# Kernel optimization log

Hardware: AMD Instinct MI355X
Metric: run time of the kernel (lower is better)

Reference implementation:

```python
import jax, jax.numpy as jnp
import numpy as np

D = 256; H = 8; DK = D // H
NA = 100000; NP_ = 100000; E = 400000
EPS = 1e-5


def _seg_softmax(s, seg, n):
    # destination-grouped (dst-normalized) edge softmax, per head
    m = jax.ops.segment_max(s, seg, num_segments=n)
    ex = jnp.exp(s - m[seg])
    den = jax.ops.segment_sum(ex, seg, num_segments=n)
    return ex / den[seg]


def setup_inputs() -> dict:
    key = jax.random.key(0)
    ks = jax.random.split(key, 16)
    sc = 1.0 / np.sqrt(D)
    sck = 1.0 / np.sqrt(DK)
    return {
        "h_author": jax.random.normal(ks[0], (NA, D), jnp.float32),
        "h_paper": jax.random.normal(ks[1], (NP_, D), jnp.float32),
        "writes_src": jax.random.randint(ks[2], (E,), 0, NA),
        "writes_dst": jax.random.randint(ks[3], (E,), 0, NP_),
        "wb_src": jax.random.randint(ks[4], (E,), 0, NP_),
        "wb_dst": jax.random.randint(ks[5], (E,), 0, NA),
        "cites_src": jax.random.randint(ks[6], (E,), 0, NP_),
        "cites_dst": jax.random.randint(ks[7], (E,), 0, NP_),
        # per-node-type linear layers, stacked on leading axis [num_node_types=2, ...]
        "Wk": jax.random.normal(ks[8], (2, D, D), jnp.float32) * sc,
        "bk": jnp.zeros((2, D), jnp.float32),
        "Wq": jax.random.normal(ks[9], (2, D, D), jnp.float32) * sc,
        "bq": jnp.zeros((2, D), jnp.float32),
        "Wv": jax.random.normal(ks[10], (2, D, D), jnp.float32) * sc,
        "bv": jnp.zeros((2, D), jnp.float32),
        "Wfc": jax.random.normal(ks[11], (2, D, D), jnp.float32) * sc,
        "bfc": jnp.zeros((2, D), jnp.float32),
        "ln_g": jnp.ones((2, D), jnp.float32),
        "ln_b": jnp.zeros((2, D), jnp.float32),
        # per-edge-type tensors [num_edge_types=3, ...]
        "att_w": jax.random.normal(ks[12], (3, H, DK, DK), jnp.float32) * sck,
        "val_w": jax.random.normal(ks[13], (3, H, DK, DK), jnp.float32) * sck,
        "canon_w": jnp.ones((3, H), jnp.float32),
        "res": jnp.ones((2,), jnp.float32),
    }


def reference(h_author, h_paper, writes_src, writes_dst, wb_src, wb_dst,
              cites_src, cites_dst, Wk, bk, Wq, bq, Wv, bv, Wfc, bfc,
              ln_g, ln_b, att_w, val_w, canon_w, res):
    sqrt_dk = np.float32(np.sqrt(DK))

    def proj(h, W, b):
        return (h @ W + b).reshape(-1, H, DK)  # [N, H, d_k]

    # node type 0 = author, 1 = paper
    k_a, v_a, q_a = proj(h_author, Wk[0], bk[0]), proj(h_author, Wv[0], bv[0]), proj(h_author, Wq[0], bq[0])
    k_p, v_p, q_p = proj(h_paper, Wk[1], bk[1]), proj(h_paper, Wv[1], bv[1]), proj(h_paper, Wq[1], bq[1])

    def etype_agg(q_d, k_s, v_s, src, dst, e, n_dst):
        ke = jnp.einsum('nhd,hde->nhe', k_s, att_w[e])
        ve = jnp.einsum('nhd,hde->nhe', v_s, val_w[e])
        score = jnp.einsum('ehd,ehd->eh', q_d[dst], ke[src]) * canon_w[e] / sqrt_dk  # [E, H]
        a = _seg_softmax(score, dst, n_dst)
        return jax.ops.segment_sum(ve[src] * a[:, :, None], dst, num_segments=n_dst)  # [N_d, H, d_k]

    agg_writes = etype_agg(q_p, k_a, v_a, writes_src, writes_dst, 0, NP_)
    agg_wb = etype_agg(q_a, k_p, v_p, wb_src, wb_dst, 1, NA)
    agg_cites = etype_agg(q_p, k_p, v_p, cites_src, cites_dst, 2, NP_)

    t_author = agg_wb                          # single incoming etype -> mean is identity
    t_paper = 0.5 * (agg_writes + agg_cites)   # cross_reducer='mean' over 2 etypes

    def node_out(t, h, nid):
        alpha = jax.nn.sigmoid(res[nid])
        hp = (t.reshape(-1, D) @ Wfc[nid] + bfc[nid]) * alpha + h * (1.0 - alpha)
        mu = hp.mean(-1, keepdims=True)
        var = ((hp - mu) ** 2).mean(-1, keepdims=True)
        return (hp - mu) / jnp.sqrt(var + EPS) * ln_g[nid] + ln_b[nid]

    return node_out(t_author, h_author, 0), node_out(t_paper, h_paper, 1)
```

## Files before the change

### kernel.cpp

```cpp
#include <hip/hip_runtime.h>
#include <hip/hip_bf16.h>
#include <math.h>

using short8  = __attribute__((ext_vector_type(8))) short;
using ushort8v = __attribute__((ext_vector_type(8))) unsigned short;
using f32x4   = __attribute__((ext_vector_type(4))) float;

__device__ __forceinline__ float bf2f(unsigned short u) {
    return __uint_as_float(((unsigned int)u) << 16);
}
__device__ __forceinline__ unsigned short f2bf(float f) {
    unsigned int x = __float_as_uint(f);
    return (unsigned short)((x + 0x7fffu + ((x >> 16) & 1u)) >> 16);
}
__device__ __forceinline__ void gll16(const void* g, void* l) {
    __builtin_amdgcn_global_load_lds(
        (const __attribute__((address_space(1))) unsigned int*)g,
        (__attribute__((address_space(3))) unsigned int*)l, 16, 0, 0);
}

__global__ __launch_bounds__(256) void build_eff_t(
    const float* __restrict__ Wk, const float* __restrict__ Wv,
    const float* __restrict__ att_w, const float* __restrict__ val_w,
    unsigned short* __restrict__ wt)
{
    int gid = blockIdx.x;
    int mat = gid >> 8, c = gid & 255;
    int e = mat >> 1, which = mat & 1;
    int ts = (e == 0) ? 0 : 1;
    int h = c >> 5, j = c & 31;
    int k = threadIdx.x;
    const float* Wsrc = (which == 0 ? Wk : Wv) + ((size_t)ts * 256 + k) * 256 + h * 32;
    const float* aw = (which == 0 ? att_w : val_w) + (size_t)((e * 8 + h) * 32) * 32 + j;
    float s = 0.f;
    #pragma unroll
    for (int d = 0; d < 32; ++d) s += Wsrc[d] * aw[d * 32];
    int slot = mat < 2 ? mat + 1 : mat + 2;
    wt[((size_t)slot * 256 + c) * 256 + k] = f2bf(s);
}

__global__ void build_eff_bias(
    const float* __restrict__ bk, const float* __restrict__ bv,
    const float* __restrict__ att_w, const float* __restrict__ val_w,
    float* __restrict__ effb)
{
    int mat = blockIdx.x;
    int c = threadIdx.x;
    int e = mat >> 1, which = mat & 1;
    int ts = (e == 0) ? 0 : 1;
    int h = c >> 5, j = c & 31;
    const float* bsrc = (which == 0 ? bk : bv) + ts * 256 + h * 32;
    const float* aw = (which == 0 ? att_w : val_w) + (size_t)((e * 8 + h) * 32) * 32 + j;
    float s = 0.f;
    #pragma unroll
    for (int d = 0; d < 32; ++d) s += bsrc[d] * aw[d * 32];
    effb[mat * 256 + c] = s;
}

__global__ void build_bias_cat(const float* __restrict__ bq,
                               const float* __restrict__ effb,
                               float* __restrict__ bc)
{
    int i = blockIdx.x * 256 + threadIdx.x;
    int seg = i >> 8, o = i & 255;
    float v;
    switch (seg) {
        case 0: v = bq[o]; break;
        case 1: v = effb[o]; break;
        case 2: v = effb[256 + o]; break;
        case 3: v = bq[256 + o]; break;
        case 4: v = effb[512 + o]; break;
        case 5: v = effb[768 + o]; break;
        case 6: v = effb[1024 + o]; break;
        default: v = effb[1280 + o]; break;
    }
    bc[i] = v;
}

__global__ __launch_bounds__(256) void transpose_cast4(
    const float* __restrict__ Wq, const float* __restrict__ Wfc,
    unsigned short* __restrict__ wt)
{
    __shared__ float tile[32][33];
    int mi = blockIdx.x >> 6;
    int bid = blockIdx.x & 63;
    const float* src; int slot;
    switch (mi) {
        case 0: src = Wq;           slot = 0; break;
        case 1: src = Wq + 65536;   slot = 3; break;
        case 2: src = Wfc;          slot = 8; break;
        default: src = Wfc + 65536; slot = 9; break;
    }
    unsigned short* dst = wt + (size_t)slot * 65536;
    int bx = bid & 7, by = bid >> 3;
    int tx = threadIdx.x & 31, ty = threadIdx.x >> 5;
    #pragma unroll
    for (int i = 0; i < 4; ++i)
        tile[ty + i * 8][tx] = src[(size_t)(by * 32 + ty + i * 8) * 256 + bx * 32 + tx];
    __syncthreads();
    #pragma unroll
    for (int i = 0; i < 4; ++i)
        dst[(size_t)(bx * 32 + ty + i * 8) * 256 + by * 32 + tx] = f2bf(tile[tx][ty + i * 8]);
}

__global__ void cast_bf16(const float* __restrict__ in, unsigned short* __restrict__ out, int n4) {
    int i = blockIdx.x * 256 + threadIdx.x;
    if (i < n4) {
        float4 v = ((const float4*)in)[i];
        ushort4 o; o.x = f2bf(v.x); o.y = f2bf(v.y); o.z = f2bf(v.z); o.w = f2bf(v.w);
        ((ushort4*)out)[i] = o;
    }
}

__global__ __launch_bounds__(256, 4) void gemm_cat(
    const unsigned short* __restrict__ A, const unsigned short* __restrict__ Wt,
    const float* __restrict__ bias, unsigned short* __restrict__ C,
    int M, int Ncat)
{
    __shared__ unsigned short As[2][128 * 32];
    __shared__ unsigned short Bs[2][128 * 32];
    int t = threadIdx.x, w = t >> 6, l = t & 63;
    int lr = l & 15, lg = l >> 4;
    int wr = w >> 1, wc = w & 1;
    int m0 = blockIdx.x * 128, n0 = blockIdx.y * 128;

    int lrow = l >> 2, lq = l & 3;
    int qsw = lq ^ ((lrow >> 1) & 3);
    int ar0 = m0 + w * 16 + lrow;        if (ar0 >= M) ar0 = M - 1;
    int ar1 = m0 + (w + 4) * 16 + lrow;  if (ar1 >= M) ar1 = M - 1;
    const unsigned short* Ap0 = A + (size_t)ar0 * 256 + qsw * 8;
    const unsigned short* Ap1 = A + (size_t)ar1 * 256 + qsw * 8;
    const unsigned short* Bp0 = Wt + (size_t)(n0 + w * 16 + lrow) * 256 + qsw * 8;
    const unsigned short* Bp1 = Wt + (size_t)(n0 + (w + 4) * 16 + lrow) * 256 + qsw * 8;

    int aswz = (lg ^ ((lr >> 1) & 3)) * 8;

    f32x4 acc[4][4] = {};

    gll16(Ap0, &As[0][(w * 16) * 32]);
    gll16(Ap1, &As[0][((w + 4) * 16) * 32]);
    gll16(Bp0, &Bs[0][(w * 16) * 32]);
    gll16(Bp1, &Bs[0][((w + 4) * 16) * 32]);
    __syncthreads();

    int cur = 0;
    for (int step = 0; step < 8; ++step) {
        if (step < 7) {
            int k0 = (step + 1) * 32;
            gll16(Ap0 + k0, &As[cur ^ 1][(w * 16) * 32]);
            gll16(Ap1 + k0, &As[cur ^ 1][((w + 4) * 16) * 32]);
            gll16(Bp0 + k0, &Bs[cur ^ 1][(w * 16) * 32]);
            gll16(Bp1 + k0, &Bs[cur ^ 1][((w + 4) * 16) * 32]);
        }
        short8 fa[4], fb[4];
        #pragma unroll
        for (int f = 0; f < 4; ++f) {
            fa[f] = *(const short8*)&As[cur][(wr * 64 + f * 16 + lr) * 32 + aswz];
            fb[f] = *(const short8*)&Bs[cur][(wc * 64 + f * 16 + lr) * 32 + aswz];
        }
        #pragma unroll
        for (int fr = 0; fr < 4; ++fr)
            #pragma unroll
            for (int fc = 0; fc < 4; ++fc)
                acc[fr][fc] = __builtin_amdgcn_mfma_f32_16x16x32_bf16(fa[fr], fb[fc], acc[fr][fc], 0, 0, 0);
        __syncthreads();
        cur ^= 1;
    }

    #pragma unroll
    for (int fr = 0; fr < 4; ++fr) {
        int row = m0 + wr * 64 + fr * 16 + lg * 4;
        #pragma unroll
        for (int fc = 0; fc < 4; ++fc) {
            int col = n0 + wc * 64 + fc * 16 + lr;
            float bv = bias[col];
            #pragma unroll
            for (int ri = 0; ri < 4; ++ri) {
                if (row + ri < M)
                    C[(size_t)(row + ri) * Ncat + col] = f2bf(acc[fr][fc][ri] + bv);
            }
        }
    }
}

__global__ __launch_bounds__(512, 2) void gemm_ln2(
    const unsigned short* __restrict__ Aa, const unsigned short* __restrict__ Ap2,
    const unsigned short* __restrict__ WtFc,
    const float* __restrict__ hA, const float* __restrict__ hP,
    const float* __restrict__ bfc, const float* __restrict__ gg,
    const float* __restrict__ bb, const float* __restrict__ res,
    float* __restrict__ out, int NA, int NP, int nbA)
{
    __shared__ unsigned short As[2][128 * 32];
    __shared__ unsigned short Bs[2][256 * 32];
    __shared__ float red_s[128][2], red_q[128][2];

    int bid = blockIdx.x;
    int isP = bid >= nbA;
    int m0 = (isP ? bid - nbA : bid) * 128;
    int M = isP ? NP : NA;
    const unsigned short* A = isP ? Ap2 : Aa;
    const float* hin = isP ? hP : hA;
    float* o = out + (isP ? (size_t)NA * 256 : 0);
    const unsigned short* Wt = WtFc + (isP ? (size_t)256 * 256 : 0);
    const float* bfcn = bfc + (isP ? 256 : 0);
    const float* gn = gg + (isP ? 256 : 0);
    const float* bn = bb + (isP ? 256 : 0);
    float alpha = 1.f / (1.f + __expf(-res[isP ? 1 : 0]));
    float beta = 1.f - alpha;

    int t = threadIdx.x, w = t >> 6, l = t & 63;
    int lr = l & 15, lg = l >> 4;
    int wr = w >> 1, wc = w & 1;

    int lrow = l >> 2, lq = l & 3;
    int qsw = lq ^ ((lrow >> 1) & 3);
    int ar = m0 + w * 16 + lrow; if (ar >= M) ar = M - 1;
    const unsigned short* Apt = A  + (size_t)ar * 256 + qsw * 8;
    const unsigned short* Bp0 = Wt + (size_t)(w * 16 + lrow) * 256 + qsw * 8;
    const unsigned short* Bp1 = Wt + (size_t)((w + 8) * 16 + lrow) * 256 + qsw * 8;

    int aswz = (lg ^ ((lr >> 1) & 3)) * 8;

    f32x4 acc[2][8] = {};

    gll16(Apt, &As[0][(w * 16) * 32]);
    gll16(Bp0, &Bs[0][(w * 16) * 32]);
    gll16(Bp1, &Bs[0][((w + 8) * 16) * 32]);
    __syncthreads();

    int cur = 0;
    for (int step = 0; step < 8; ++step) {
        if (step < 7) {
            int k0 = (step + 1) * 32;
            gll16(Apt + k0, &As[cur ^ 1][(w * 16) * 32]);
            gll16(Bp0 + k0, &Bs[cur ^ 1][(w * 16) * 32]);
            gll16(Bp1 + k0, &Bs[cur ^ 1][((w + 8) * 16) * 32]);
        }
        short8 fa[2], fb[8];
        #pragma unroll
        for (int f = 0; f < 2; ++f)
            fa[f] = *(const short8*)&As[cur][(wr * 32 + f * 16 + lr) * 32 + aswz];
        #pragma unroll
        for (int f = 0; f < 8; ++f)
            fb[f] = *(const short8*)&Bs[cur][(wc * 128 + f * 16 + lr) * 32 + aswz];
        #pragma unroll
        for (int fr = 0; fr < 2; ++fr)
            #pragma unroll
            for (int fc = 0; fc < 8; ++fc)
                acc[fr][fc] = __builtin_amdgcn_mfma_f32_16x16x32_bf16(fa[fr], fb[fc], acc[fr][fc], 0, 0, 0);
        __syncthreads();
        cur ^= 1;
    }

    #pragma unroll
    for (int fr = 0; fr < 2; ++fr) {
        #pragma unroll
        for (int ri = 0; ri < 4; ++ri) {
            int rloc = wr * 32 + fr * 16 + lg * 4 + ri;
            int row = m0 + rloc;
            int rowc = row < M ? row : M - 1;
            float ps = 0.f, pq = 0.f;
            #pragma unroll
            for (int fc = 0; fc < 8; ++fc) {
                int col = wc * 128 + fc * 16 + lr;
                float hp = alpha * (acc[fr][fc][ri] + bfcn[col])
                         + beta * hin[(size_t)rowc * 256 + col];
                acc[fr][fc][ri] = hp;
                ps += hp;
                pq += hp * hp;
            }
            #pragma unroll
            for (int m = 1; m < 16; m <<= 1) {
                ps += __shfl_xor(ps, m);
                pq += __shfl_xor(pq, m);
            }
            if (lr == 0) { red_s[rloc][wc] = ps; red_q[rloc][wc] = pq; }
        }
    }
    __syncthreads();
    #pragma unroll
    for (int fr = 0; fr < 2; ++fr) {
        #pragma unroll
        for (int ri = 0; ri < 4; ++ri) {
            int rloc = wr * 32 + fr * 16 + lg * 4 + ri;
            int row = m0 + rloc;
            float s = red_s[rloc][0] + red_s[rloc][1];
            float q = red_q[rloc][0] + red_q[rloc][1];
            float mu = s * (1.f / 256.f);
            float var = q * (1.f / 256.f) - mu * mu;
            float rstd = rsqrtf(var + 1e-5f);
            if (row < M) {
                #pragma unroll
                for (int fc = 0; fc < 8; ++fc) {
                    int col = wc * 128 + fc * 16 + lr;
                    o[(size_t)row * 256 + col] =
                        (acc[fr][fc][ri] - mu) * rstd * gn[col] + bn[col];
                }
            }
        }
    }
}

__global__ void k_hist3(const int* __restrict__ d0, const int* __restrict__ d1,
                        const int* __restrict__ d2, int E0, int E1, int E2,
                        int nb0, int nb01, int P, int* __restrict__ cnt)
{
    int bid = blockIdx.x;
    const int* d; int E, eb, base;
    if (bid < nb0)       { d = d0; E = E0; eb = bid;        base = 0; }
    else if (bid < nb01) { d = d1; E = E1; eb = bid - nb0;  base = P; }
    else                 { d = d2; E = E2; eb = bid - nb01; base = 2 * P; }
    int e = eb * 256 + threadIdx.x;
    if (e < E) atomicAdd(&cnt[base + d[e]], 1);
}

__global__ __launch_bounds__(256) void k_scan1(
    const int* __restrict__ cnt, int* __restrict__ offs, int* __restrict__ blksum, int N)
{
    __shared__ int sm[256];
    int t = threadIdx.x, i = blockIdx.x * 256 + t;
    int x = (i < N) ? cnt[i] : 0;
    sm[t] = x; __syncthreads();
    int v = x;
    #pragma unroll
    for (int off = 1; off < 256; off <<= 1) {
        int y = (t >= off) ? sm[t - off] : 0;
        __syncthreads();
        v += y; sm[t] = v;
        __syncthreads();
    }
    if (i < N) offs[i] = v - x;
    if (t == 255) blksum[blockIdx.x] = v;
}

__global__ __launch_bounds__(512) void k_scan2s(int* __restrict__ blksum, int nbseg) {
    __shared__ int sm[512];
    int t = threadIdx.x;
    int* bs = blksum + blockIdx.x * nbseg;
    int x = (t < nbseg) ? bs[t] : 0;
    sm[t] = x; __syncthreads();
    int v = x;
    #pragma unroll
    for (int off = 1; off < 512; off <<= 1) {
        int y = (t >= off) ? sm[t - off] : 0;
        __syncthreads();
        v += y; sm[t] = v;
        __syncthreads();
    }
    if (t < nbseg) bs[t] = v - x;
}

__global__ void k_scan3(int* __restrict__ offs, int* __restrict__ cursor,
                        const int* __restrict__ blksum, int N)
{
    int i = blockIdx.x * 256 + threadIdx.x;
    if (i < N) {
        int v = offs[i] + blksum[i >> 8];
        offs[i] = v;
        cursor[i] = v;
    }
}

__global__ void k_scatter3(const int* __restrict__ s0, const int* __restrict__ d0,
                           const int* __restrict__ s1, const int* __restrict__ d1,
                           const int* __restrict__ s2, const int* __restrict__ d2,
                           int E0, int E1, int E2, int nb0, int nb01, int P,
                           int* __restrict__ cursor, int* __restrict__ ssrc)
{
    int bid = blockIdx.x;
    const int* s; const int* d; int E, eb, bn, be;
    if (bid < nb0)       { s = s0; d = d0; E = E0; eb = bid;        bn = 0;     be = 0; }
    else if (bid < nb01) { s = s1; d = d1; E = E1; eb = bid - nb0;  bn = P;     be = E0; }
    else                 { s = s2; d = d2; E = E2; eb = bid - nb01; bn = 2 * P; be = E0 + E1; }
    int e = eb * 256 + threadIdx.x;
    if (e < E) {
        int pos = atomicAdd(&cursor[bn + d[e]], 1);
        ssrc[be + pos] = s[e];
    }
}

__device__ __forceinline__ void seg_agg8(
    int base, int deg, const int* __restrict__ ssrc,
    const unsigned short* __restrict__ ke, int ks,
    const unsigned short* __restrict__ ve, int vs,
    const float* qf, float cw, int sl, int half,
    float* o)
{
    float den = 0.f;
    float acc[8] = {0.f,0.f,0.f,0.f,0.f,0.f,0.f,0.f};
    for (int i = 0; i < deg; i += 2) {
        int idx = i + half;
        if (idx < deg) {
            int s = ssrc[base + idx];
            ushort8v kv = *(const ushort8v*)(ke + (size_t)s * ks + sl * 8);
            float p = qf[0] * bf2f(kv[0]) + qf[1] * bf2f(kv[1])
                    + qf[2] * bf2f(kv[2]) + qf[3] * bf2f(kv[3])
                    + qf[4] * bf2f(kv[4]) + qf[5] * bf2f(kv[5])
                    + qf[6] * bf2f(kv[6]) + qf[7] * bf2f(kv[7]);
            p += __shfl_xor(p, 1);
            p += __shfl_xor(p, 2);
            float ex = __expf(p * cw);
            ushort8v vv = *(const ushort8v*)(ve + (size_t)s * vs + sl * 8);
            den += ex;
            #pragma unroll
            for (int j = 0; j < 8; ++j) acc[j] += ex * bf2f(vv[j]);
        }
    }
    den += __shfl_xor(den, 32);
    #pragma unroll
    for (int j = 0; j < 8; ++j) acc[j] += __shfl_xor(acc[j], 32);
    float r = den > 0.f ? 1.f / den : 0.f;
    #pragma unroll
    for (int j = 0; j < 8; ++j) o[j] = acc[j] * r;
}

__global__ __launch_bounds__(256) void agg_all(
    const int* __restrict__ cnt, const int* __restrict__ offs,
    const int* __restrict__ ssrc, int P, int E0, int E1,
    const unsigned short* __restrict__ qkv_a,
    const unsigned short* __restrict__ qkv_p,
    const float* __restrict__ canon, float rsdk,
    unsigned short* __restrict__ agg_w, unsigned short* __restrict__ agg_wb,
    int NP, int NA)
{
    int wave = threadIdx.x >> 6, lane = threadIdx.x & 63;
    int sl = lane & 31, half = lane >> 5;
    int g = blockIdx.x * 4 + wave;
    int h = sl >> 2;
    if (g < NP) {
        const unsigned short* qrow = qkv_p + (size_t)g * 1280;
        ushort8v q8 = *(const ushort8v*)(qrow + sl * 8);
        float qf[8];
        #pragma unroll
        for (int j = 0; j < 8; ++j) qf[j] = bf2f(q8[j]);
        float a[8], b[8];
        seg_agg8(offs[g], cnt[g], ssrc,
                 qkv_a + 256, 768, qkv_a + 512, 768,
                 qf, canon[h] * rsdk, sl, half, a);
        seg_agg8(offs[2 * P + g], cnt[2 * P + g], ssrc + (E0 + E1),
                 qkv_p + 768, 1280, qkv_p + 1024, 1280,
                 qf, canon[16 + h] * rsdk, sl, half, b);
        if (half == 0) {
            ushort8v o8;
            #pragma unroll
            for (int j = 0; j < 8; ++j) o8[j] = f2bf(0.5f * (a[j] + b[j]));
            *(ushort8v*)(agg_w + (size_t)g * 256 + sl * 8) = o8;
        }
    } else if (g < NP + NA) {
        int n = g - NP;
        const unsigned short* qrow = qkv_a + (size_t)n * 768;
        ushort8v q8 = *(const ushort8v*)(qrow + sl * 8);
        float qf[8];
        #pragma unroll
        for (int j = 0; j < 8; ++j) qf[j] = bf2f(q8[j]);
        float a[8];
        seg_agg8(offs[P + n], cnt[P + n], ssrc + E0,
                 qkv_p + 256, 1280, qkv_p + 512, 1280,
                 qf, canon[8 + h] * rsdk, sl, half, a);
        if (half == 0) {
            ushort8v o8;
            #pragma unroll
            for (int j = 0; j < 8; ++j) o8[j] = f2bf(a[j]);
            *(ushort8v*)(agg_wb + (size_t)n * 256 + sl * 8) = o8;
        }
    }
}

extern "C" void kernel_launch(void* const* d_in, const int* in_sizes, int n_in,
                              void* d_out, int out_size, void* d_ws, size_t ws_size,
                              hipStream_t stream)
{
    const float* h_a   = (const float*)d_in[0];
    const float* h_p   = (const float*)d_in[1];
    const int* w_src   = (const int*)d_in[2];
    const int* w_dst   = (const int*)d_in[3];
    const int* wb_src  = (const int*)d_in[4];
    const int* wb_dst  = (const int*)d_in[5];
    const int* c_src   = (const int*)d_in[6];
    const int* c_dst   = (const int*)d_in[7];
    const float* Wk    = (const float*)d_in[8];
    const float* bk    = (const float*)d_in[9];
    const float* Wq    = (const float*)d_in[10];
    const float* bq    = (const float*)d_in[11];
    const float* Wv    = (const float*)d_in[12];
    const float* bv    = (const float*)d_in[13];
    const float* Wfc   = (const float*)d_in[14];
    const float* bfc   = (const float*)d_in[15];
    const float* ln_g  = (const float*)d_in[16];
    const float* ln_b  = (const float*)d_in[17];
    const float* att_w = (const float*)d_in[18];
    const float* val_w = (const float*)d_in[19];
    const float* canon = (const float*)d_in[20];
    const float* res   = (const float*)d_in[21];

    const int NA = in_sizes[0] / 256;
    const int NP = in_sizes[1] / 256;
    const int E0 = in_sizes[2];
    const int E1 = in_sizes[4];
    const int E2 = in_sizes[6];
    const int Nmax = NA > NP ? NA : NP;
    const int P = ((Nmax + 255) / 256) * 256;
    const int nbseg = P / 256;

    char* p = (char*)d_ws;
    auto alloc = [&](size_t bytes) -> char* {
        char* r = p;
        p += (bytes + 255) & ~(size_t)255;
        return r;
    };
    unsigned short* wt = (unsigned short*)alloc((size_t)10 * 65536 * 2);
    float* eff_b = (float*)alloc(6 * 256 * 4);
    float* bias_cat = (float*)alloc(2048 * 4);
    unsigned short* qkv_a = (unsigned short*)alloc((size_t)NA * 768 * 2);
    unsigned short* qkv_p = (unsigned short*)alloc((size_t)NP * 1280 * 2);
    unsigned short* agg_w  = (unsigned short*)alloc((size_t)NP * 256 * 2);
    unsigned short* agg_wb = (unsigned short*)alloc((size_t)NA * 256 * 2);
    int* cnt    = (int*)alloc((size_t)3 * P * 4);
    int* offs   = (int*)alloc((size_t)3 * P * 4);
    int* cursor = (int*)alloc((size_t)3 * P * 4);
    int* blksum = (int*)alloc((size_t)3 * nbseg * 4);
    int* ssrc   = (int*)alloc((size_t)(E0 + E1 + E2) * 4);

    unsigned short* ha_bf = (unsigned short*)d_out;
    unsigned short* hp_bf = ha_bf + (size_t)NA * 256;

    const float rsdk = 0.17677669529663687f;

    build_eff_t<<<1536, 256, 0, stream>>>(Wk, Wv, att_w, val_w, wt);
    build_eff_bias<<<6, 256, 0, stream>>>(bk, bv, att_w, val_w, eff_b);
    build_bias_cat<<<8, 256, 0, stream>>>(bq, eff_b, bias_cat);
    transpose_cast4<<<256, 256, 0, stream>>>(Wq, Wfc, wt);
    cast_bf16<<<(NA * 64 + 255) / 256, 256, 0, stream>>>(h_a, ha_bf, NA * 64);
    cast_bf16<<<(NP * 64 + 255) / 256, 256, 0, stream>>>(h_p, hp_bf, NP * 64);

    hipMemsetAsync(cnt, 0, (size_t)3 * P * 4, stream);
    int nb0 = (E0 + 255) / 256, nb1 = (E1 + 255) / 256, nb2 = (E2 + 255) / 256;
    k_hist3<<<nb0 + nb1 + nb2, 256, 0, stream>>>(w_dst, wb_dst, c_dst, E0, E1, E2,
                                                 nb0, nb0 + nb1, P, cnt);
    k_scan1<<<3 * nbseg, 256, 0, stream>>>(cnt, offs, blksum, 3 * P);
    k_scan2s<<<3, 512, 0, stream>>>(blksum, nbseg);
    k_scan3<<<3 * nbseg, 256, 0, stream>>>(offs, cursor, blksum, 3 * P);
    k_scatter3<<<nb0 + nb1 + nb2, 256, 0, stream>>>(w_src, w_dst, wb_src, wb_dst,
                                                    c_src, c_dst, E0, E1, E2,
                                                    nb0, nb0 + nb1, P, cursor, ssrc);

    int gA = (NA + 127) / 128, gP = (NP + 127) / 128;
    gemm_cat<<<dim3(gA, 6), 256, 0, stream>>>(ha_bf, wt, bias_cat, qkv_a, NA, 768);
    gemm_cat<<<dim3(gP, 10), 256, 0, stream>>>(hp_bf, wt + (size_t)768 * 256,
                                               bias_cat + 768, qkv_p, NP, 1280);

    agg_all<<<(NP + NA + 3) / 4, 256, 0, stream>>>(cnt, offs, ssrc, P, E0, E1,
                                                   qkv_a, qkv_p, canon, rsdk,
                                                   agg_w, agg_wb, NP, NA);

    gemm_ln2<<<gA + gP, 512, 0, stream>>>(agg_wb, agg_w, wt + (size_t)2048 * 256,
                                          h_a, h_p, bfc, ln_g, ln_b, res,
                                          (float*)d_out, NA, NP, gA);
}
```

Before: 835.3 us.

## Split edge aggregation into separate score and apply kernels, merge bf16 casts

The fused softmax-aggregate kernel is split in two. The first kernel gathers keys, computes the exponentiated scores and per-destination denominators, and stores them to new workspace buffers. The second kernel gathers values and accumulates the normalized weighted sum. Separating the two gathers may reduce register pressure and let each random-access stream run on its own, at the cost of an extra launch and the write and read of an exp buffer (E×8 floats). The two bf16 cast launches are also merged into one.

```diff
diff --git a/kernel.cpp b/kernel.cpp
--- a/kernel.cpp
+++ b/kernel.cpp
@@ -103,12 +103,20 @@
         dst[(size_t)(bx * 32 + ty + i * 8) * 256 + by * 32 + tx] = f2bf(tile[tx][ty + i * 8]);
 }
 
-__global__ void cast_bf16(const float* __restrict__ in, unsigned short* __restrict__ out, int n4) {
+__global__ void cast_bf16_2(const float* __restrict__ a, const float* __restrict__ b,
+                            unsigned short* __restrict__ oa, unsigned short* __restrict__ ob,
+                            int n4a, int n4b)
+{
     int i = blockIdx.x * 256 + threadIdx.x;
-    if (i < n4) {
-        float4 v = ((const float4*)in)[i];
+    if (i < n4a) {
+        float4 v = ((const float4*)a)[i];
         ushort4 o; o.x = f2bf(v.x); o.y = f2bf(v.y); o.z = f2bf(v.z); o.w = f2bf(v.w);
-        ((ushort4*)out)[i] = o;
+        ((ushort4*)oa)[i] = o;
+    } else if (i - n4a < n4b) {
+        int j = i - n4a;
+        float4 v = ((const float4*)b)[j];
+        ushort4 o; o.x = f2bf(v.x); o.y = f2bf(v.y); o.z = f2bf(v.z); o.w = f2bf(v.w);
+        ((ushort4*)ob)[j] = o;
     }
 }
 
@@ -380,48 +388,42 @@
     }
 }
 
-__device__ __forceinline__ void seg_agg8(
+__device__ __forceinline__ float dot8(const float* qf, ushort8v kv) {
+    return qf[0] * bf2f(kv[0]) + qf[1] * bf2f(kv[1])
+         + qf[2] * bf2f(kv[2]) + qf[3] * bf2f(kv[3])
+         + qf[4] * bf2f(kv[4]) + qf[5] * bf2f(kv[5])
+         + qf[6] * bf2f(kv[6]) + qf[7] * bf2f(kv[7]);
+}
+
+__device__ __forceinline__ void score_seg(
     int base, int deg, const int* __restrict__ ssrc,
     const unsigned short* __restrict__ ke, int ks,
-    const unsigned short* __restrict__ ve, int vs,
     const float* qf, float cw, int sl, int half,
-    float* o)
-{
-    float den = 0.f;
-    float acc[8] = {0.f,0.f,0.f,0.f,0.f,0.f,0.f,0.f};
-    for (int i = 0; i < deg; i += 2) {
-        int idx = i + half;
-        if (idx < deg) {
-            int s = ssrc[base + idx];
-            ushort8v kv = *(const ushort8v*)(ke + (size_t)s * ks + sl * 8);
-            float p = qf[0] * bf2f(kv[0]) + qf[1] * bf2f(kv[1])
-                    + qf[2] * bf2f(kv[2]) + qf[3] * bf2f(kv[3])
-                    + qf[4] * bf2f(kv[4]) + qf[5] * bf2f(kv[5])
-                    + qf[6] * bf2f(kv[6]) + qf[7] * bf2f(kv[7]);
-            p += __shfl_xor(p, 1);
-            p += __shfl_xor(p, 2);
-            float ex = __expf(p * cw);
-            ushort8v vv = *(const ushort8v*)(ve + (size_t)s * vs + sl * 8);
-            den += ex;
-            #pragma unroll
-            for (int j = 0; j < 8; ++j) acc[j] += ex * bf2f(vv[j]);
-        }
-    }
-    den += __shfl_xor(den, 32);
-    #pragma unroll
-    for (int j = 0; j < 8; ++j) acc[j] += __shfl_xor(acc[j], 32);
-    float r = den > 0.f ? 1.f / den : 0.f;
-    #pragma unroll
-    for (int j = 0; j < 8; ++j) o[j] = acc[j] * r;
-}
-
-__global__ __launch_bounds__(256) void agg_all(
+    float* __restrict__ exb, float* __restrict__ den8)
+{
+    int h = sl >> 2;
+    float dn = 0.f;
+    for (int i = half; i < deg; i += 2) {
+        int s = ssrc[base + i];
+        ushort8v kv = *(const ushort8v*)(ke + (size_t)s * ks + sl * 8);
+        float p = dot8(qf, kv);
+        p += __shfl_xor(p, 1);
+        p += __shfl_xor(p, 2);
+        float ex = __expf(p * cw);
+        dn += ex;
+        if ((sl & 3) == 0) exb[(size_t)(base + i) * 8 + h] = ex;
+    }
+    dn += __shfl_xor(dn, 32);
+    if (half == 0 && (sl & 3) == 0) den8[h] = dn;
+}
+
+__global__ __launch_bounds__(256) void agg_score(
     const int* __restrict__ cnt, const int* __restrict__ offs,
     const int* __restrict__ ssrc, int P, int E0, int E1,
     const unsigned short* __restrict__ qkv_a,
     const unsigned short* __restrict__ qkv_p,
     const float* __restrict__ canon, float rsdk,
-    unsigned short* __restrict__ agg_w, unsigned short* __restrict__ agg_wb,
+    float* __restrict__ exbuf, float* __restrict__ den,
     int NP, int NA)
 {
     int wave = threadIdx.x >> 6, lane = threadIdx.x & 63;
@@ -429,18 +431,70 @@
     int g = blockIdx.x * 4 + wave;
     int h = sl >> 2;
     if (g < NP) {
-        const unsigned short* qrow = qkv_p + (size_t)g * 1280;
-        ushort8v q8 = *(const ushort8v*)(qrow + sl * 8);
+        const ushort8v* qp8 = (const ushort8v*)(qkv_p + (size_t)g * 1280);
+        ushort8v q8 = __builtin_nontemporal_load(qp8 + sl);
         float qf[8];
         #pragma unroll
         for (int j = 0; j < 8; ++j) qf[j] = bf2f(q8[j]);
+        score_seg(offs[g], cnt[g], ssrc, qkv_a + 256, 768,
+                  qf, canon[h] * rsdk, sl, half, exbuf, den + (size_t)g * 8);
+        score_seg(offs[2 * P + g], cnt[2 * P + g], ssrc + (E0 + E1), qkv_p + 768, 1280,
+                  qf, canon[16 + h] * rsdk, sl, half,
+                  exbuf + (size_t)(E0 + E1) * 8, den + ((size_t)2 * P + g) * 8);
+    } else if (g < NP + NA) {
+        int n = g - NP;
+        const ushort8v* qa8 = (const ushort8v*)(qkv_a + (size_t)n * 768);
+        ushort8v q8 = __builtin_nontemporal_load(qa8 + sl);
+        float qf[8];
+        #pragma unroll
+        for (int j = 0; j < 8; ++j) qf[j] = bf2f(q8[j]);
+        score_seg(offs[P + n], cnt[P + n], ssrc + E0, qkv_p + 256, 1280,
+                  qf, canon[8 + h] * rsdk, sl, half,
+                  exbuf + (size_t)E0 * 8, den + ((size_t)P + n) * 8);
+    }
+}
+
+__device__ __forceinline__ void apply_seg(
+    int base, int deg, const int* __restrict__ ssrc,
+    const unsigned short* __restrict__ ve, int vs,
+    const float* __restrict__ exb, const float* __restrict__ den8,
+    int sl, int half, float* o)
+{
+    int h = sl >> 2;
+    float acc[8] = {0.f,0.f,0.f,0.f,0.f,0.f,0.f,0.f};
+    for (int i = half; i < deg; i += 2) {
+        int s = ssrc[base + i];
+        float ex = exb[(size_t)(base + i) * 8 + h];
+        ushort8v vv = *(const ushort8v*)(ve + (size_t)s * vs + sl * 8);
+        #pragma unroll
+        for (int j = 0; j < 8; ++j) acc[j] += ex * bf2f(vv[j]);
+    }
+    #pragma unroll
+    for (int j = 0; j < 8; ++j) acc[j] += __shfl_xor(acc[j], 32);
+    float dn = den8[h];
+    float r = dn > 0.f ? 1.f / dn : 0.f;
+    #pragma unroll
+    for (int j = 0; j < 8; ++j) o[j] = acc[j] * r;
+}
+
+__global__ __launch_bounds__(256) void agg_apply(
+    const int* __restrict__ cnt, const int* __restrict__ offs,
+    const int* __restrict__ ssrc, int P, int E0, int E1,
+    const unsigned short* __restrict__ qkv_a,
+    const unsigned short* __restrict__ qkv_p,
+    const float* __restrict__ exbuf, const float* __restrict__ den,
+    unsigned short* __restrict__ agg_w, unsigned short* __restrict__ agg_wb,
+    int NP, int NA)
+{
+    int wave = threadIdx.x >> 6, lane = threadIdx.x & 63;
+    int sl = lane & 31, half = lane >> 5;
+    int g = blockIdx.x * 4 + wave;
+    if (g < NP) {
         float a[8], b[8];
-        seg_agg8(offs[g], cnt[g], ssrc,
-                 qkv_a + 256, 768, qkv_a + 512, 768,
-                 qf, canon[h] * rsdk, sl, half, a);
-        seg_agg8(offs[2 * P + g], cnt[2 * P + g], ssrc + (E0 + E1),
-                 qkv_p + 768, 1280, qkv_p + 1024, 1280,
-                 qf, canon[16 + h] * rsdk, sl, half, b);
+        apply_seg(offs[g], cnt[g], ssrc, qkv_a + 512, 768,
+                  exbuf, den + (size_t)g * 8, sl, half, a);
+        apply_seg(offs[2 * P + g], cnt[2 * P + g], ssrc + (E0 + E1), qkv_p + 1024, 1280,
+                  exbuf + (size_t)(E0 + E1) * 8, den + ((size_t)2 * P + g) * 8, sl, half, b);
         if (half == 0) {
             ushort8v o8;
             #pragma unroll
@@ -449,15 +503,9 @@
         }
     } else if (g < NP + NA) {
         int n = g - NP;
-        const unsigned short* qrow = qkv_a + (size_t)n * 768;
-        ushort8v q8 = *(const ushort8v*)(qrow + sl * 8);
-        float qf[8];
-        #pragma unroll
-        for (int j = 0; j < 8; ++j) qf[j] = bf2f(q8[j]);
         float a[8];
-        seg_agg8(offs[P + n], cnt[P + n], ssrc + E0,
-                 qkv_p + 256, 1280, qkv_p + 512, 1280,
-                 qf, canon[8 + h] * rsdk, sl, half, a);
+        apply_seg(offs[P + n], cnt[P + n], ssrc + E0, qkv_p + 512, 1280,
+                  exbuf + (size_t)E0 * 8, den + ((size_t)P + n) * 8, sl, half, a);
         if (half == 0) {
             ushort8v o8;
             #pragma unroll
@@ -502,6 +550,7 @@
     const int Nmax = NA > NP ? NA : NP;
     const int P = ((Nmax + 255) / 256) * 256;
     const int nbseg = P / 256;
+    const int Etot = E0 + E1 + E2;
 
     char* p = (char*)d_ws;
     auto alloc = [&](size_t bytes) -> char* {
@@ -520,7 +569,9 @@
     int* offs   = (int*)alloc((size_t)3 * P * 4);
     int* cursor = (int*)alloc((size_t)3 * P * 4);
     int* blksum = (int*)alloc((size_t)3 * nbseg * 4);
-    int* ssrc   = (int*)alloc((size_t)(E0 + E1 + E2) * 4);
+    int* ssrc   = (int*)alloc((size_t)Etot * 4);
+    float* exbuf = (float*)alloc((size_t)Etot * 8 * 4);
+    float* den   = (float*)alloc((size_t)3 * P * 8 * 4);
 
     unsigned short* ha_bf = (unsigned short*)d_out;
     unsigned short* hp_bf = ha_bf + (size_t)NA * 256;
@@ -531,8 +582,8 @@
     build_eff_bias<<<6, 256, 0, stream>>>(bk, bv, att_w, val_w, eff_b);
     build_bias_cat<<<8, 256, 0, stream>>>(bq, eff_b, bias_cat);
     transpose_cast4<<<256, 256, 0, stream>>>(Wq, Wfc, wt);
-    cast_bf16<<<(NA * 64 + 255) / 256, 256, 0, stream>>>(h_a, ha_bf, NA * 64);
-    cast_bf16<<<(NP * 64 + 255) / 256, 256, 0, stream>>>(h_p, hp_bf, NP * 64);
+    cast_bf16_2<<<(NA * 64 + NP * 64 + 255) / 256, 256, 0, stream>>>(
+        h_a, h_p, ha_bf, hp_bf, NA * 64, NP * 64);
 
     hipMemsetAsync(cnt, 0, (size_t)3 * P * 4, stream);
     int nb0 = (E0 + 255) / 256, nb1 = (E1 + 255) / 256, nb2 = (E2 + 255) / 256;
@@ -550,9 +601,11 @@
     gemm_cat<<<dim3(gP, 10), 256, 0, stream>>>(hp_bf, wt + (size_t)768 * 256,
                                                bias_cat + 768, qkv_p, NP, 1280);
 
-    agg_all<<<(NP + NA + 3) / 4, 256, 0, stream>>>(cnt, offs, ssrc, P, E0, E1,
-                                                   qkv_a, qkv_p, canon, rsdk,
-                                                   agg_w, agg_wb, NP, NA);
+    int gagg = (NP + NA + 3) / 4;
+    agg_score<<<gagg, 256, 0, stream>>>(cnt, offs, ssrc, P, E0, E1,
+                                        qkv_a, qkv_p, canon, rsdk, exbuf, den, NP, NA);
+    agg_apply<<<gagg, 256, 0, stream>>>(cnt, offs, ssrc, P, E0, E1,
+                                        qkv_a, qkv_p, exbuf, den, agg_w, agg_wb, NP, NA);
 
     gemm_ln2<<<gA + gP, 512, 0, stream>>>(agg_wb, agg_w, wt + (size_t)2048 * 256,
                                           h_a, h_p, bfc, ln_g, ln_b, res,
```

Result: slower. 960.1 us (+14.9%).
